# Optimization experiments

Hardware: AMD Instinct MI355X
Metric: run time of the kernel (lower is better)

## Reference

```python
import math
import jax, jax.numpy as jnp
import numpy as np

B, N, D_IN, D_OUT = 8, 2048, 768, 768

def setup_inputs() -> dict:
    key = jax.random.key(0)
    k1, k2, k3 = jax.random.split(key, 3)
    x = jax.random.normal(k1, (B, N, D_IN), dtype=jnp.float32)
    W_qkv = jax.random.normal(k2, (D_IN, 3 * D_OUT), dtype=jnp.float32) * (1.0 / math.sqrt(D_IN))
    b_qkv = jax.random.normal(k3, (3 * D_OUT,), dtype=jnp.float32) * 0.02
    return {"x": x, "W_qkv": W_qkv, "b_qkv": b_qkv}

def reference(x, W_qkv, b_qkv):
    d_out = D_OUT
    # fused QKV projection: [B, N, 3*d_out]
    qkv = jnp.einsum('bnd,de->bne', x, W_qkv) + b_qkv
    q = qkv[:, :, :d_out]
    k = qkv[:, :, d_out:2 * d_out]
    v = qkv[:, :, 2 * d_out:3 * d_out]
    scale = 1.0 / math.sqrt(d_out)
    # scores: [B, N, N]
    scores = jnp.einsum('bqd,bkd->bqk', q, k) * scale
    attn = jax.nn.softmax(scores, axis=-1)
    # context: [B, N, d_out]
    context = jnp.einsum('bqk,bkd->bqd', attn, v)
    return context
```

## Files before the change

kernel.cpp:

```cpp
#include <hip/hip_runtime.h>
#include <hip/hip_bf16.h>

typedef __attribute__((ext_vector_type(8))) short short8;
typedef __attribute__((ext_vector_type(4))) float floatx4;

#define BATCH 8
#define SEQ 2048
#define DMODEL 768
#define NQKV 2304
#define SCALE 0.03608439182435161f

__device__ __forceinline__ ushort f2bf(float f) {
    union { float f; uint u; } in; in.f = f;
    uint u = in.u;
    return (ushort)((u + 0x7FFFu + ((u >> 16) & 1u)) >> 16);
}
__device__ __forceinline__ float bf2f(ushort h) {
    union { uint u; float f; } o; o.u = ((uint)h) << 16;
    return o.f;
}

__device__ __forceinline__ void async_copy16(void* lds_uniform, const void* gaddr) {
    __builtin_amdgcn_global_load_lds(
        (const __attribute__((address_space(1))) void*)gaddr,
        (__attribute__((address_space(3))) void*)lds_uniform,
        16, 0, 0);
}

#define BARRIER() asm volatile("s_barrier" ::: "memory")
#define LGKM0()   do { asm volatile("s_waitcnt lgkmcnt(0)" ::: "memory"); \
                       __builtin_amdgcn_sched_barrier(0); } while (0)
#define LGKM_HINT() asm volatile("s_waitcnt lgkmcnt(8)" ::: "memory")
#define VMCNT(n)  asm volatile("s_waitcnt vmcnt(" #n ")" ::: "memory")

template<int MODE, int KT>
__global__ __launch_bounds__(512, 2) void gemm8(
    const ushort* __restrict__ A, const ushort* __restrict__ B,
    const float* __restrict__ bias,
    void* __restrict__ out0, void* __restrict__ out1, void* __restrict__ out2,
    int lda, int ldb)
{
    extern __shared__ __align__(16) ushort lds[];
    const int tid  = threadIdx.x;
    const int w    = tid >> 6, lane = tid & 63;
    const int wr   = w >> 2,  wc   = w & 3;
    const int lr   = lane & 15, kg = lane >> 4;
    const int srow = lane >> 3;
    const int scc  = (lane & 7) ^ srow;

    const int m0 = blockIdx.x * 256, n0 = blockIdx.y * 256;
    const ushort* Abase;
    const ushort* Bbase;
    if (MODE == 0) {
        Abase = A + (size_t)m0 * lda;
        Bbase = B + (size_t)n0 * ldb;
    } else if (MODE == 1) {
        const int b = blockIdx.z;
        Abase = A + ((size_t)(b * SEQ + m0)) * lda;
        Bbase = B + ((size_t)(b * SEQ + n0)) * ldb;
    } else {
        const int b = blockIdx.z;
        Abase = A + (size_t)b * SEQ * SEQ + (size_t)m0 * lda;
        Bbase = B + (size_t)b * DMODEL * SEQ + (size_t)n0 * ldb;
    }

    const ushort* At[2] = { lds,         lds + 32768 };
    const ushort* Bt[2] = { lds + 16384, lds + 49152 };

    #define STG(tile, mat, half) do { if ((tile) < KT) {                          \
        ushort* sb_ = lds + (((tile) & 1) ? 32768 : 0) + ((mat) ? 16384 : 0);     \
        const ushort* g_ = (mat) ? Bbase : Abase;                                 \
        const size_t ld_ = (mat) ? (size_t)ldb : (size_t)lda;                     \
        const int k0_ = (tile) << 6;                                              \
        _Pragma("unroll")                                                         \
        for (int t_ = 0; t_ < 2; ++t_) {                                          \
            const int c8_ = (mat) ? ((w & 3) + ((w >> 2) << 3) + (t_ << 4) + ((half) << 2)) \
                                  : (w + (t_ << 4) + ((half) << 3));              \
            const int row_ = (c8_ << 3) + srow;                                   \
            async_copy16(sb_ + c8_ * 512, g_ + (size_t)row_ * ld_ + k0_ + scc * 8); \
        } } } while (0)

    short8 af[4][2], bf[4][2];
    floatx4 acc[8][4] = {};

    #define LDFRAG(tp, row, c) \
        (*reinterpret_cast<const short8*>(&(tp)[((row) << 6) + ((((c) ^ ((row) & 7))) << 3)]))

    #define READ_A(bufi, mh) do {                                                 \
        _Pragma("unroll") for (int mf_ = 0; mf_ < 4; ++mf_)                       \
        _Pragma("unroll") for (int kk_ = 0; kk_ < 2; ++kk_)                       \
            af[mf_][kk_] = LDFRAG(At[bufi], wr * 128 + ((mh) * 4 + mf_) * 16 + lr, kk_ * 4 + kg); \
    } while (0)
    #define READ_B(bufi, nh) do {                                                 \
        _Pragma("unroll") for (int nf_ = 0; nf_ < 2; ++nf_)                       \
        _Pragma("unroll") for (int kk_ = 0; kk_ < 2; ++kk_)                       \
            bf[(nh) * 2 + nf_][kk_] = LDFRAG(Bt[bufi], wc * 64 + ((nh) * 2 + nf_) * 16 + lr, kk_ * 4 + kg); \
    } while (0)
    #define MFMA_Q(mh, nh) do {                                                   \
        __builtin_amdgcn_s_setprio(1);                                            \
        _Pragma("unroll") for (int mf_ = 0; mf_ < 4; ++mf_)                       \
        _Pragma("unroll") for (int nf_ = 0; nf_ < 2; ++nf_)                       \
        _Pragma("unroll") for (int kk_ = 0; kk_ < 2; ++kk_)                       \
            acc[(mh) * 4 + mf_][(nh) * 2 + nf_] = __builtin_amdgcn_mfma_f32_16x16x32_bf16( \
                af[mf_][kk_], bf[(nh) * 2 + nf_][kk_], acc[(mh) * 4 + mf_][(nh) * 2 + nf_], 0, 0, 0); \
        __builtin_amdgcn_s_setprio(0);                                            \
    } while (0)

    STG(0, 0, 0); STG(0, 1, 0); STG(0, 1, 1); STG(0, 0, 1);
    STG(1, 0, 0); STG(1, 1, 0); STG(1, 1, 1);
    VMCNT(6);
    BARRIER();

    #pragma unroll 1
    for (int it = 0; it < KT / 2; ++it) {
        const int t = 2 * it;
        const bool lastit = (it == KT / 2 - 1);
        READ_A(0, 0); READ_B(0, 0);
        STG(t + 1, 0, 1);
        LGKM_HINT();
        BARRIER(); LGKM0();
        MFMA_Q(0, 0);
        BARRIER();
        READ_B(0, 1);
        STG(t + 2, 0, 0);
        BARRIER(); LGKM0();
        MFMA_Q(0, 1);
        BARRIER();
        READ_A(0, 1);
        STG(t + 2, 1, 0);
        BARRIER(); LGKM0();
        MFMA_Q(1, 0);
        BARRIER();
        STG(t + 2, 1, 1);
        BARRIER();
        MFMA_Q(1, 1);
        if (lastit) { VMCNT(0); } else { VMCNT(6); }
        BARRIER();
        READ_A(1, 0); READ_B(1, 0);
        STG(t + 2, 0, 1);
        LGKM_HINT();
        BARRIER(); LGKM0();
        MFMA_Q(0, 0);
        BARRIER();
        READ_B(1, 1);
        STG(t + 3, 0, 0);
        BARRIER(); LGKM0();
        MFMA_Q(0, 1);
        BARRIER();
        READ_A(1, 1);
        STG(t + 3, 1, 0);
        BARRIER(); LGKM0();
        MFMA_Q(1, 0);
        BARRIER();
        STG(t + 3, 1, 1);
        BARRIER();
        MFMA_Q(1, 1);
        VMCNT(6);
        BARRIER();
    }

    {
        float* scr = reinterpret_cast<float*>(reinterpret_cast<char*>(lds) + (size_t)w * 9216);
        const int mrow = m0 + wr * 128;
        const int ncol = n0 + wc * 64;
        #pragma unroll
        for (int mh = 0; mh < 2; ++mh) {
            #pragma unroll
            for (int np = 0; np < 2; ++np) {
                #pragma unroll
                for (int mf = 0; mf < 4; ++mf)
                    #pragma unroll
                    for (int nf2 = 0; nf2 < 2; ++nf2) {
                        const floatx4 v = acc[mh * 4 + mf][np * 2 + nf2];
                        *reinterpret_cast<floatx4*>(
                            &scr[(nf2 * 16 + lr) * 68 + mf * 16 + kg * 4]) = v;
                    }
                asm volatile("s_waitcnt lgkmcnt(0)" ::: "memory");
                __builtin_amdgcn_sched_barrier(0);

                if (MODE == 2) {
                    float* Ob = (float*)out0 + (size_t)blockIdx.z * SEQ * DMODEL;
                    const int c4 = (lane & 7) * 4;
                    #pragma unroll
                    for (int p = 0; p < 8; ++p) {
                        const int row = p * 8 + (lane >> 3);
                        float4 v;
                        v.x = scr[(c4 + 0) * 68 + row];
                        v.y = scr[(c4 + 1) * 68 + row];
                        v.z = scr[(c4 + 2) * 68 + row];
                        v.w = scr[(c4 + 3) * 68 + row];
                        *reinterpret_cast<float4*>(
                            &Ob[(size_t)(mrow + mh * 64 + row) * DMODEL + ncol + np * 32 + c4]) = v;
                    }
                } else {
                    const int c8 = (lane & 3) * 8;
                    const int e0 = ncol + np * 32 + c8;
                    ushort* dst; int ec; float mul;
                    float bs[8] = {0, 0, 0, 0, 0, 0, 0, 0};
                    if (MODE == 0) {
                        const bool isQ = e0 < DMODEL, isK = !isQ && (e0 < 2 * DMODEL);
                        dst = isQ ? (ushort*)out0 : (isK ? (ushort*)out1 : (ushort*)out2);
                        ec  = isQ ? e0 : (isK ? e0 - DMODEL : e0 - 2 * DMODEL);
                        mul = isQ ? SCALE : 1.0f;
                        const float4 b0 = *reinterpret_cast<const float4*>(&bias[e0]);
                        const float4 b1 = *reinterpret_cast<const float4*>(&bias[e0 + 4]);
                        bs[0] = b0.x * mul; bs[1] = b0.y * mul;
                        bs[2] = b0.z * mul; bs[3] = b0.w * mul;
                        bs[4] = b1.x * mul; bs[5] = b1.y * mul;
                        bs[6] = b1.z * mul; bs[7] = b1.w * mul;
                    } else {
                        dst = (ushort*)out0 + (size_t)blockIdx.z * SEQ * SEQ;
                        ec = e0; mul = 1.0f;
                    }
                    const size_t ostride = (MODE == 0) ? (size_t)DMODEL : (size_t)SEQ;
                    #pragma unroll
                    for (int p = 0; p < 4; ++p) {
                        const int row = p * 16 + (lane >> 2);
                        short8 o;
                        #pragma unroll
                        for (int j = 0; j < 8; ++j) {
                            const float f = scr[(c8 + j) * 68 + row] * mul + bs[j];
                            o[j] = (short)f2bf(f);
                        }
                        *reinterpret_cast<short8*>(
                            &dst[(size_t)(mrow + mh * 64 + row) * ostride + ec]) = o;
                    }
                }
                asm volatile("s_waitcnt lgkmcnt(0)" ::: "memory");
                __builtin_amdgcn_sched_barrier(0);
            }
        }
    }
    #undef STG
    #undef LDFRAG
    #undef READ_A
    #undef READ_B
    #undef MFMA_Q
}

__global__ __launch_bounds__(256) void convert_x(const float* __restrict__ X,
                                                 ushort* __restrict__ Xb) {
    const int total = (BATCH * SEQ * DMODEL) / 8;
    for (int i = blockIdx.x * 256 + threadIdx.x; i < total; i += gridDim.x * 256) {
        const float4 v0 = reinterpret_cast<const float4*>(X)[(size_t)i * 2];
        const float4 v1 = reinterpret_cast<const float4*>(X)[(size_t)i * 2 + 1];
        uint4 u;
        u.x = (uint)f2bf(v0.x) | ((uint)f2bf(v0.y) << 16);
        u.y = (uint)f2bf(v0.z) | ((uint)f2bf(v0.w) << 16);
        u.z = (uint)f2bf(v1.x) | ((uint)f2bf(v1.y) << 16);
        u.w = (uint)f2bf(v1.z) | ((uint)f2bf(v1.w) << 16);
        reinterpret_cast<uint4*>(Xb)[i] = u;
    }
}

__global__ __launch_bounds__(256) void convert_wt(const float* __restrict__ W,
                                                  ushort* __restrict__ Wt) {
    __shared__ float tile[32][33];
    const int n0 = blockIdx.x * 32, k0 = blockIdx.y * 32;
    const int tx = threadIdx.x & 31, ty = threadIdx.x >> 5;
    #pragma unroll
    for (int i = 0; i < 32; i += 8)
        tile[ty + i][tx] = W[(size_t)(k0 + ty + i) * NQKV + n0 + tx];
    __syncthreads();
    #pragma unroll
    for (int i = 0; i < 32; i += 8)
        Wt[(size_t)(n0 + ty + i) * DMODEL + k0 + tx] = f2bf(tile[tx][ty + i]);
}

__global__ __launch_bounds__(256) void transpose_v(const ushort* __restrict__ Vb,
                                                   ushort* __restrict__ Vt) {
    __shared__ ushort tile[32][33];
    const int b = blockIdx.z;
    const int n0 = blockIdx.x * 32, d0 = blockIdx.y * 32;
    const ushort* src = Vb + (size_t)b * SEQ * DMODEL;
    ushort* dst = Vt + (size_t)b * DMODEL * SEQ;
    const int tx = threadIdx.x & 31, ty = threadIdx.x >> 5;
    #pragma unroll
    for (int i = 0; i < 32; i += 8)
        tile[ty + i][tx] = src[(size_t)(n0 + ty + i) * DMODEL + d0 + tx];
    __syncthreads();
    #pragma unroll
    for (int i = 0; i < 32; i += 8)
        dst[(size_t)(d0 + ty + i) * SEQ + n0 + tx] = tile[tx][ty + i];
}

__global__ __launch_bounds__(256) void softmax_rows(ushort* __restrict__ S) {
    const int row = blockIdx.x;
    ushort* p = S + (size_t)row * SEQ;
    const int tid = threadIdx.x;
    const int wave = tid >> 6, lane = tid & 63;

    short8 v8 = *reinterpret_cast<const short8*>(p + tid * 8);
    float v[8];
    #pragma unroll
    for (int j = 0; j < 8; ++j) v[j] = bf2f((ushort)v8[j]);
    float mx = v[0];
    #pragma unroll
    for (int j = 1; j < 8; ++j) mx = fmaxf(mx, v[j]);
    #pragma unroll
    for (int off = 32; off >= 1; off >>= 1) mx = fmaxf(mx, __shfl_xor(mx, off));
    __shared__ float redm[4], reds[4];
    if (lane == 0) redm[wave] = mx;
    __syncthreads();
    mx = fmaxf(fmaxf(redm[0], redm[1]), fmaxf(redm[2], redm[3]));

    float e[8], s = 0.f;
    #pragma unroll
    for (int j = 0; j < 8; ++j) { e[j] = __expf(v[j] - mx); s += e[j]; }
    #pragma unroll
    for (int off = 32; off >= 1; off >>= 1) s += __shfl_xor(s, off);
    if (lane == 0) reds[wave] = s;
    __syncthreads();
    s = reds[0] + reds[1] + reds[2] + reds[3];
    float inv = 1.f / s;

    short8 o;
    #pragma unroll
    for (int j = 0; j < 8; ++j) o[j] = (short)f2bf(e[j] * inv);
    *reinterpret_cast<short8*>(p + tid * 8) = o;
}

extern "C" void kernel_launch(void* const* d_in, const int* in_sizes, int n_in,
                              void* d_out, int out_size, void* d_ws, size_t ws_size,
                              hipStream_t stream) {
    const float* X    = (const float*)d_in[0];
    const float* W    = (const float*)d_in[1];
    const float* bias = (const float*)d_in[2];
    float* Out = (float*)d_out;

    char* ws = (char*)d_ws;
    ushort* S  = (ushort*)ws;
    ushort* Xb = (ushort*)ws;
    ushort* Wt = (ushort*)(ws + (size_t)BATCH * SEQ * DMODEL * 2);
    ushort* Qs = (ushort*)(ws + (size_t)BATCH * SEQ * SEQ * 2);
    ushort* Kb = Qs + (size_t)BATCH * SEQ * DMODEL;
    ushort* Vb = Kb + (size_t)BATCH * SEQ * DMODEL;
    ushort* Vt = Vb + (size_t)BATCH * SEQ * DMODEL;

    const int LDSB = 131072;
    (void)hipFuncSetAttribute((const void*)gemm8<0, 12>,
                              hipFuncAttributeMaxDynamicSharedMemorySize, LDSB);
    (void)hipFuncSetAttribute((const void*)gemm8<1, 12>,
                              hipFuncAttributeMaxDynamicSharedMemorySize, LDSB);
    (void)hipFuncSetAttribute((const void*)gemm8<2, 32>,
                              hipFuncAttributeMaxDynamicSharedMemorySize, LDSB);

    convert_x<<<2048, 256, 0, stream>>>(X, Xb);
    convert_wt<<<dim3(NQKV / 32, DMODEL / 32), 256, 0, stream>>>(W, Wt);
    gemm8<0, 12><<<dim3(64, 9), 512, LDSB, stream>>>(
        Xb, Wt, bias, Qs, Kb, Vb, DMODEL, DMODEL);
    transpose_v<<<dim3(SEQ / 32, DMODEL / 32, BATCH), 256, 0, stream>>>(Vb, Vt);
    gemm8<1, 12><<<dim3(8, 8, 8), 512, LDSB, stream>>>(
        Qs, Kb, nullptr, S, nullptr, nullptr, DMODEL, DMODEL);
    softmax_rows<<<BATCH * SEQ, 256, 0, stream>>>(S);
    gemm8<2, 32><<<dim3(8, 3, 8), 512, LDSB, stream>>>(
        S, Vt, nullptr, Out, nullptr, nullptr, SEQ, SEQ);
}
```

Baseline: 258.9 us.

## Fuse V transpose into QKV GEMM epilogue and re-layout LDS scratch

Blocks of the QKV projection GEMM that produce V columns now write V transposed straight from the accumulators into the Vt buffer. This removes the separate transpose_v kernel and the round trip of V through global memory. The LDS scratch used by the other epilogues changes from a column-major layout to a row-major one with stride 36, so each read becomes one vectorized float4 load, while each write becomes four scalar stores. The direct Vt stores are narrow 8-byte writes scattered across rows, which may coalesce poorly.

```diff
diff --git a/kernel.cpp b/kernel.cpp
--- a/kernel.cpp
+++ b/kernel.cpp
@@ -159,10 +159,30 @@
         BARRIER();
     }
 
-    {
+    const int mrow = m0 + wr * 128;
+    const int ncol = n0 + wc * 64;
+
+    if (MODE == 0 && blockIdx.y >= 6) {
+        ushort* Vt = (ushort*)out2;
+        const int bIdx = m0 >> 11;
+        const int ns0  = m0 & 2047;
+        #pragma unroll
+        for (int nf = 0; nf < 4; ++nf) {
+            const int e = ncol + nf * 16 + lr;
+            const int d = e - 2 * DMODEL;
+            const float bv = bias[e];
+            ushort* vrow = Vt + ((size_t)bIdx * DMODEL + d) * SEQ + ns0;
+            #pragma unroll
+            for (int a = 0; a < 8; ++a) {
+                const floatx4 v = acc[a][nf];
+                uint2 u;
+                u.x = (uint)f2bf(v[0] + bv) | ((uint)f2bf(v[1] + bv) << 16);
+                u.y = (uint)f2bf(v[2] + bv) | ((uint)f2bf(v[3] + bv) << 16);
+                *reinterpret_cast<uint2*>(vrow + wr * 128 + a * 16 + kg * 4) = u;
+            }
+        }
+    } else {
         float* scr = reinterpret_cast<float*>(reinterpret_cast<char*>(lds) + (size_t)w * 9216);
-        const int mrow = m0 + wr * 128;
-        const int ncol = n0 + wc * 64;
         #pragma unroll
         for (int mh = 0; mh < 2; ++mh) {
             #pragma unroll
@@ -172,8 +192,9 @@
                     #pragma unroll
                     for (int nf2 = 0; nf2 < 2; ++nf2) {
                         const floatx4 v = acc[mh * 4 + mf][np * 2 + nf2];
-                        *reinterpret_cast<floatx4*>(
-                            &scr[(nf2 * 16 + lr) * 68 + mf * 16 + kg * 4]) = v;
+                        #pragma unroll
+                        for (int r = 0; r < 4; ++r)
+                            scr[(mf * 16 + kg * 4 + r) * 36 + nf2 * 16 + lr] = v[r];
                     }
                 asm volatile("s_waitcnt lgkmcnt(0)" ::: "memory");
                 __builtin_amdgcn_sched_barrier(0);
@@ -184,11 +205,7 @@
                     #pragma unroll
                     for (int p = 0; p < 8; ++p) {
                         const int row = p * 8 + (lane >> 3);
-                        float4 v;
-                        v.x = scr[(c4 + 0) * 68 + row];
-                        v.y = scr[(c4 + 1) * 68 + row];
-                        v.z = scr[(c4 + 2) * 68 + row];
-                        v.w = scr[(c4 + 3) * 68 + row];
+                        const float4 v = *reinterpret_cast<const float4*>(&scr[row * 36 + c4]);
                         *reinterpret_cast<float4*>(
                             &Ob[(size_t)(mrow + mh * 64 + row) * DMODEL + ncol + np * 32 + c4]) = v;
                     }
@@ -198,9 +215,9 @@
                     ushort* dst; int ec; float mul;
                     float bs[8] = {0, 0, 0, 0, 0, 0, 0, 0};
                     if (MODE == 0) {
-                        const bool isQ = e0 < DMODEL, isK = !isQ && (e0 < 2 * DMODEL);
-                        dst = isQ ? (ushort*)out0 : (isK ? (ushort*)out1 : (ushort*)out2);
-                        ec  = isQ ? e0 : (isK ? e0 - DMODEL : e0 - 2 * DMODEL);
+                        const bool isQ = e0 < DMODEL;
+                        dst = isQ ? (ushort*)out0 : (ushort*)out1;
+                        ec  = isQ ? e0 : e0 - DMODEL;
                         mul = isQ ? SCALE : 1.0f;
                         const float4 b0 = *reinterpret_cast<const float4*>(&bias[e0]);
                         const float4 b1 = *reinterpret_cast<const float4*>(&bias[e0 + 4]);
@@ -216,12 +233,17 @@
                     #pragma unroll
                     for (int p = 0; p < 4; ++p) {
                         const int row = p * 16 + (lane >> 2);
+                        const float4 lo = *reinterpret_cast<const float4*>(&scr[row * 36 + c8]);
+                        const float4 hi = *reinterpret_cast<const float4*>(&scr[row * 36 + c8 + 4]);
                         short8 o;
-                        #pragma unroll
-                        for (int j = 0; j < 8; ++j) {
-                            const float f = scr[(c8 + j) * 68 + row] * mul + bs[j];
-                            o[j] = (short)f2bf(f);
-                        }
+                        o[0] = (short)f2bf(lo.x * mul + bs[0]);
+                        o[1] = (short)f2bf(lo.y * mul + bs[1]);
+                        o[2] = (short)f2bf(lo.z * mul + bs[2]);
+                        o[3] = (short)f2bf(lo.w * mul + bs[3]);
+                        o[4] = (short)f2bf(hi.x * mul + bs[4]);
+                        o[5] = (short)f2bf(hi.y * mul + bs[5]);
+                        o[6] = (short)f2bf(hi.z * mul + bs[6]);
+                        o[7] = (short)f2bf(hi.w * mul + bs[7]);
                         *reinterpret_cast<short8*>(
                             &dst[(size_t)(mrow + mh * 64 + row) * ostride + ec]) = o;
                     }
@@ -267,23 +289,6 @@
         Wt[(size_t)(n0 + ty + i) * DMODEL + k0 + tx] = f2bf(tile[tx][ty + i]);
 }
 
-__global__ __launch_bounds__(256) void transpose_v(const ushort* __restrict__ Vb,
-                                                   ushort* __restrict__ Vt) {
-    __shared__ ushort tile[32][33];
-    const int b = blockIdx.z;
-    const int n0 = blockIdx.x * 32, d0 = blockIdx.y * 32;
-    const ushort* src = Vb + (size_t)b * SEQ * DMODEL;
-    ushort* dst = Vt + (size_t)b * DMODEL * SEQ;
-    const int tx = threadIdx.x & 31, ty = threadIdx.x >> 5;
-    #pragma unroll
-    for (int i = 0; i < 32; i += 8)
-        tile[ty + i][tx] = src[(size_t)(n0 + ty + i) * DMODEL + d0 + tx];
-    __syncthreads();
-    #pragma unroll
-    for (int i = 0; i < 32; i += 8)
-        dst[(size_t)(d0 + ty + i) * SEQ + n0 + tx] = tile[tx][ty + i];
-}
-
 __global__ __launch_bounds__(256) void softmax_rows(ushort* __restrict__ S) {
     const int row = blockIdx.x;
     ushort* p = S + (size_t)row * SEQ;
@@ -334,8 +339,7 @@
     ushort* Wt = (ushort*)(ws + (size_t)BATCH * SEQ * DMODEL * 2);
     ushort* Qs = (ushort*)(ws + (size_t)BATCH * SEQ * SEQ * 2);
     ushort* Kb = Qs + (size_t)BATCH * SEQ * DMODEL;
-    ushort* Vb = Kb + (size_t)BATCH * SEQ * DMODEL;
-    ushort* Vt = Vb + (size_t)BATCH * SEQ * DMODEL;
+    ushort* Vt = Kb + (size_t)BATCH * SEQ * DMODEL;
 
     const int LDSB = 131072;
     (void)hipFuncSetAttribute((const void*)gemm8<0, 12>,
@@ -348,8 +352,7 @@
     convert_x<<<2048, 256, 0, stream>>>(X, Xb);
     convert_wt<<<dim3(NQKV / 32, DMODEL / 32), 256, 0, stream>>>(W, Wt);
     gemm8<0, 12><<<dim3(64, 9), 512, LDSB, stream>>>(
-        Xb, Wt, bias, Qs, Kb, Vb, DMODEL, DMODEL);
-    transpose_v<<<dim3(SEQ / 32, DMODEL / 32, BATCH), 256, 0, stream>>>(Vb, Vt);
+        Xb, Wt, bias, Qs, Kb, Vt, DMODEL, DMODEL);
     gemm8<1, 12><<<dim3(8, 8, 8), 512, LDSB, stream>>>(
         Qs, Kb, nullptr, S, nullptr, nullptr, DMODEL, DMODEL);
     softmax_rows<<<BATCH * SEQ, 256, 0, stream>>>(S);
```

New measurement: 243.9 us. 1.06x faster.
